# Optimization experiments

Measured on AMD Instinct MI355X. Metric: run time of the kernel, lower is better.

The kernel has to match this reference:

```python
import jax, jax.numpy as jnp
import numpy as np

B, S, U, M = 4096, 64, 128, 32
ODE_UNFOLDS = 6
EPS = 1e-08

def _uniform(k, shape, lo, hi):
    return jax.random.uniform(k, shape, jnp.float32, lo, hi)

def setup_inputs() -> dict:
    key = jax.random.key(0)
    ks = jax.random.split(key, 16)
    return {
        "inputs": jax.random.normal(ks[0], (B, S), jnp.float32),
        "state": jax.random.normal(ks[1], (B, U), jnp.float32),
        "gleak": _uniform(ks[2], (U,), 0.001, 1.0),
        "vleak": _uniform(ks[3], (U,), -0.2, 0.2),
        "cm": _uniform(ks[4], (U,), 0.4, 0.6),
        "sigma": _uniform(ks[5], (U, U), 3.0, 8.0),
        "mu": _uniform(ks[6], (U, U), 0.3, 0.8),
        "w": _uniform(ks[7], (U, U), 0.001, 1.0),
        "erev": jnp.sign(jax.random.normal(ks[8], (U, U), jnp.float32)),
        "sensory_sigma": _uniform(ks[9], (S, U), 3.0, 8.0),
        "sensory_mu": _uniform(ks[10], (S, U), 0.3, 0.8),
        "sensory_w": _uniform(ks[11], (S, U), 0.001, 1.0),
        "sensory_erev": jnp.sign(jax.random.normal(ks[12], (S, U), jnp.float32)),
        "sparsity_mask": (jax.random.uniform(ks[13], (U, U)) < 0.5).astype(jnp.float32),
        "sensory_sparsity_mask": (jax.random.uniform(ks[14], (S, U)) < 0.5).astype(jnp.float32),
        "input_w": jnp.ones((S,), jnp.float32),
        "input_b": jnp.zeros((S,), jnp.float32),
        "output_w": jnp.ones((M,), jnp.float32),
        "output_b": jnp.zeros((M,), jnp.float32),
    }

def reference(inputs, state, gleak, vleak, cm, sigma, mu, w, erev,
              sensory_sigma, sensory_mu, sensory_w, sensory_erev,
              sparsity_mask, sensory_sparsity_mask,
              input_w, input_b, output_w, output_b):
    # input mapping (affine)
    x = inputs * input_w + input_b                       # [B,S]
    # sensory synapse activation: [B,S,U]
    sens_act = (sensory_w * sensory_sparsity_mask) * jax.nn.sigmoid(
        sensory_sigma * (x[:, :, None] - sensory_mu))
    w_num_sensory = jnp.sum(sens_act * sensory_erev, axis=1)   # [B,U]
    w_den_sensory = jnp.sum(sens_act, axis=1)                  # [B,U]

    wm = w * sparsity_mask                                     # masked weights [U,U]
    wme = wm * erev                                            # weights*erev   [U,U]
    cm_t = cm * ODE_UNFOLDS                                    # cm / (1/unfolds)
    leak = gleak * vleak

    v = state
    for _ in range(ODE_UNFOLDS):
        sig = jax.nn.sigmoid(sigma * (v[:, :, None] - mu))     # [B,U,U] (src,dst)
        w_num = jnp.einsum('bsu,su->bu', sig, wme) + w_num_sensory
        w_den = jnp.einsum('bsu,su->bu', sig, wm) + w_den_sensory
        v = (cm_t * v + leak + w_num) / (cm_t + gleak + w_den + EPS)

    out = v[:, :M] * output_w + output_b                       # motor slice + affine
    return out, v
```

## Files before the change

kernel.cpp:

```cpp
#include <hip/hip_runtime.h>
#include <hip/hip_fp16.h>

typedef unsigned short u16;
typedef unsigned int   u32;

#define B_TOTAL 4096
#define ROWS    16
#define NU      128
#define NS      64
#define NM      32
#define UNFOLDS 6
#define LOG2E   1.44269504088896340736f

__device__ __forceinline__ float bf2f(u16 v) {
  return __uint_as_float(((u32)v) << 16);
}
__device__ __forceinline__ u16 f2bf(float f) {
  u32 x = __float_as_uint(f);
  return (u16)((x + 0x7fffu + ((x >> 16) & 1u)) >> 16);
}

template<bool BF16>
__device__ __forceinline__ float LD(const void* p, int i) {
  if (BF16) return bf2f(((const u16*)p)[i]);
  return ((const float*)p)[i];
}

__device__ __forceinline__ float rdlane(float v, int lane) {
  return __int_as_float(__builtin_amdgcn_readlane(__float_as_int(v), lane));
}

__device__ __forceinline__ u32 pk(float a, float b) {
  __half2 h = __halves2half2(__float2half_rn(a), __float2half_rn(b));
  return __builtin_bit_cast(u32, h);
}

__device__ __forceinline__ void step(u32 a0, u32 a1, u32 wv, float vj,
                                     float& n0, float& d0, float& n1, float& d1) {
  float t0, t1, q, aw;
  asm("v_fma_mix_f32 %[t0], %[vj], %[a0], %[a1] op_sel:[0,0,0] op_sel_hi:[0,1,1]\n\t"
      "v_fma_mix_f32 %[t1], %[vj], %[a0], %[a1] op_sel:[0,1,1] op_sel_hi:[0,1,1]\n\t"
      "v_exp_f32 %[t0], %[t0]\n\t"
      "v_exp_f32 %[t1], %[t1]\n\t"
      "v_add_f32 %[t0], 1.0, %[t0]\n\t"
      "v_add_f32 %[t1], 1.0, %[t1]\n\t"
      "v_mul_f32 %[q], %[t0], %[t1]\n\t"
      "v_rcp_f32 %[q], %[q]\n\t"
      "v_and_b32 %[aw], 0x7fff7fff, %[w]\n\t"
      "v_mul_f32 %[t1], %[t1], %[q]\n\t"
      "v_mul_f32 %[t0], %[t0], %[q]\n\t"
      "v_fma_mix_f32 %[n0], %[t1], %[w],  %[n0] op_sel:[0,0,0] op_sel_hi:[0,1,0]\n\t"
      "v_fma_mix_f32 %[d0], %[t1], %[aw], %[d0] op_sel:[0,0,0] op_sel_hi:[0,1,0]\n\t"
      "v_fma_mix_f32 %[n1], %[t0], %[w],  %[n1] op_sel:[0,1,0] op_sel_hi:[0,1,0]\n\t"
      "v_fma_mix_f32 %[d1], %[t0], %[aw], %[d1] op_sel:[0,1,0] op_sel_hi:[0,1,0]"
      : [n0] "+v"(n0), [d0] "+v"(d0), [n1] "+v"(n1), [d1] "+v"(d1),
        [t0] "=&v"(t0), [t1] "=&v"(t1), [q] "=&v"(q), [aw] "=&v"(aw)
      : [vj] "v"(vj), [a0] "v"(a0), [a1] "v"(a1), [w] "v"(wv));
}

template<bool BF16>
__device__ __forceinline__ void body(
    const void* g_in, const void* g_state, const void* g_gleak, const void* g_vleak,
    const void* g_cm, const void* g_sigma, const void* g_mu, const void* g_w,
    const void* g_erev, const void* g_ssig, const void* g_smu, const void* g_sw,
    const void* g_serev, const void* g_mask, const void* g_smask,
    const void* g_iw, const void* g_ib, const void* g_ow, const void* g_ob,
    void* g_out,
    uint2* smA, u32* smW, uint2* smA2, u32* smW2)
{
  const int tid = threadIdx.x;
  const int b0  = blockIdx.x * ROWS;

  #pragma unroll 2
  for (int e = tid; e < NU * 64; e += 1024) {
    int j = e >> 6, l = e & 63;
    int i0 = j * NU + l, i1 = i0 + 64;
    float sl0 = LD<BF16>(g_sigma, i0) * LOG2E, sl1 = LD<BF16>(g_sigma, i1) * LOG2E;
    float ms0 = LD<BF16>(g_mu, i0) * sl0,      ms1 = LD<BF16>(g_mu, i1) * sl1;
    smA[e] = make_uint2(pk(-sl0, -sl1), pk(ms0, ms1));
    float w0 = LD<BF16>(g_w, i0) * LD<BF16>(g_mask, i0) * LD<BF16>(g_erev, i0);
    float w1 = LD<BF16>(g_w, i1) * LD<BF16>(g_mask, i1) * LD<BF16>(g_erev, i1);
    smW[e] = pk(w0, w1);
  }
  #pragma unroll 2
  for (int e = tid; e < NS * 64; e += 1024) {
    int s = e >> 6, l = e & 63;
    int i0 = s * NU + l, i1 = i0 + 64;
    float sl0 = LD<BF16>(g_ssig, i0) * LOG2E, sl1 = LD<BF16>(g_ssig, i1) * LOG2E;
    float ms0 = LD<BF16>(g_smu, i0) * sl0,    ms1 = LD<BF16>(g_smu, i1) * sl1;
    smA2[e] = make_uint2(pk(-sl0, -sl1), pk(ms0, ms1));
    float w0 = LD<BF16>(g_sw, i0) * LD<BF16>(g_smask, i0) * LD<BF16>(g_serev, i0);
    float w1 = LD<BF16>(g_sw, i1) * LD<BF16>(g_smask, i1) * LD<BF16>(g_serev, i1);
    smW2[e] = pk(w0, w1);
  }
  __syncthreads();

  const int r  = tid >> 6;
  const int u0 = tid & 63;
  const int u1 = u0 + 64;
  const int b  = b0 + r;

  float x_lane = LD<BF16>(g_in, b * NS + u0) * LD<BF16>(g_iw, u0) + LD<BF16>(g_ib, u0);
  float v0 = LD<BF16>(g_state, b * NU + u0);
  float v1 = LD<BF16>(g_state, b * NU + u1);
  const float gl0 = LD<BF16>(g_gleak, u0), gl1 = LD<BF16>(g_gleak, u1);
  const float lk0 = gl0 * LD<BF16>(g_vleak, u0);
  const float lk1 = gl1 * LD<BF16>(g_vleak, u1);
  const float cm0 = LD<BF16>(g_cm, u0) * (float)UNFOLDS;
  const float cm1 = LD<BF16>(g_cm, u1) * (float)UNFOLDS;

  const uint2* pA  = smA  + u0;
  const u32*   pW  = smW  + u0;
  const uint2* pA2 = smA2 + u0;
  const u32*   pW2 = smW2 + u0;

  float ns0 = 0.f, ds0 = 0.f, ns1 = 0.f, ds1 = 0.f;
  #pragma unroll 4
  for (int s = 0; s < NS; ++s) {
    float xs = rdlane(x_lane, s);
    uint2 a = pA2[s * 64];
    step(a.x, a.y, pW2[s * 64], xs, ns0, ds0, ns1, ds1);
  }

  #pragma unroll 1
  for (int it = 0; it < UNFOLDS; ++it) {
    float n0 = ns0, d0 = ds0, n1 = ns1, d1 = ds1;
    #pragma unroll 4
    for (int j = 0; j < 64; ++j) {
      float vj = rdlane(v0, j);
      uint2 a = pA[j * 64];
      step(a.x, a.y, pW[j * 64], vj, n0, d0, n1, d1);
    }
    #pragma unroll 4
    for (int j = 0; j < 64; ++j) {
      float vj = rdlane(v1, j);
      uint2 a = pA[(j + 64) * 64];
      step(a.x, a.y, pW[(j + 64) * 64], vj, n0, d0, n1, d1);
    }
    v0 = fmaf(cm0, v0, lk0 + n0) * __builtin_amdgcn_rcpf(cm0 + gl0 + d0 + 1e-8f);
    v1 = fmaf(cm1, v1, lk1 + n1) * __builtin_amdgcn_rcpf(cm1 + gl1 + d1 + 1e-8f);
  }

  if (BF16) {
    u16* om = (u16*)g_out;
    u16* ov = om + B_TOTAL * NM;
    ov[b * NU + u0] = f2bf(v0);
    ov[b * NU + u1] = f2bf(v1);
    if (u0 < NM)
      om[b * NM + u0] = f2bf(fmaf(v0, LD<true>(g_ow, u0), LD<true>(g_ob, u0)));
  } else {
    float* om = (float*)g_out;
    float* ov = om + B_TOTAL * NM;
    ov[b * NU + u0] = v0;
    ov[b * NU + u1] = v1;
    if (u0 < NM)
      om[b * NM + u0] = fmaf(v0, LD<false>(g_ow, u0), LD<false>(g_ob, u0));
  }
}

__global__ __launch_bounds__(1024, 4) void ltc_kernel(
    const void* g_in, const void* g_state, const void* g_gleak, const void* g_vleak,
    const void* g_cm, const void* g_sigma, const void* g_mu, const void* g_w,
    const void* g_erev, const void* g_ssig, const void* g_smu, const void* g_sw,
    const void* g_serev, const void* g_mask, const void* g_smask,
    const void* g_iw, const void* g_ib, const void* g_ow, const void* g_ob,
    void* g_out)
{
  __shared__ uint2 smA [NU * 64];
  __shared__ u32   smW [NU * 64];
  __shared__ uint2 smA2[NS * 64];
  __shared__ u32   smW2[NS * 64];

  const u16* sg = (const u16*)g_sigma;
  int cnt = 0;
  #pragma unroll
  for (int i = 0; i < 32; ++i) {
    float f = bf2f(sg[2 * i]);
    cnt += (f >= 2.0f && f <= 16.0f) ? 1 : 0;
  }
  if (cnt >= 24)
    body<true >(g_in, g_state, g_gleak, g_vleak, g_cm, g_sigma, g_mu, g_w, g_erev,
                g_ssig, g_smu, g_sw, g_serev, g_mask, g_smask,
                g_iw, g_ib, g_ow, g_ob, g_out, smA, smW, smA2, smW2);
  else
    body<false>(g_in, g_state, g_gleak, g_vleak, g_cm, g_sigma, g_mu, g_w, g_erev,
                g_ssig, g_smu, g_sw, g_serev, g_mask, g_smask,
                g_iw, g_ib, g_ow, g_ob, g_out, smA, smW, smA2, smW2);
}

extern "C" void kernel_launch(void* const* d_in, const int* in_sizes, int n_in,
                              void* d_out, int out_size, void* d_ws, size_t ws_size,
                              hipStream_t stream) {
  (void)in_sizes; (void)n_in; (void)out_size; (void)d_ws; (void)ws_size;
  dim3 grid(B_TOTAL / ROWS);
  dim3 block(1024);
  hipLaunchKernelGGL(ltc_kernel, grid, block, 0, stream,
                     d_in[0], d_in[1], d_in[2], d_in[3], d_in[4],
                     d_in[5], d_in[6], d_in[7], d_in[8],
                     d_in[9], d_in[10], d_in[11], d_in[12],
                     d_in[13], d_in[14], d_in[15], d_in[16],
                     d_in[17], d_in[18], d_out);
}
```

Measured before the change: 231.7 us.

## Interleave synapse params into uint4 LDS records and reuse buffer for sensory phase

Packs the slope, offset and weight half2 values of each synapse into one 16-byte LDS record, so each step does a single 128-bit LDS load instead of an 8-byte load plus a 4-byte load. The sensory and recurrent tables now share one buffer: the sensory table is built, consumed, then overwritten by the recurrent table, with an extra barrier between. Unroll factors rise to 8. LDS drops from 144KB to 128KB, though the padding word wastes a quarter of the bandwidth; the sensory compute no longer overlaps the recurrent table build.

```diff
diff --git a/kernel.cpp b/kernel.cpp
--- a/kernel.cpp
+++ b/kernel.cpp
@@ -66,39 +66,27 @@
     const void* g_serev, const void* g_mask, const void* g_smask,
     const void* g_iw, const void* g_ib, const void* g_ow, const void* g_ob,
     void* g_out,
-    uint2* smA, u32* smW, uint2* smA2, u32* smW2)
+    uint4* smR)
 {
   const int tid = threadIdx.x;
   const int b0  = blockIdx.x * ROWS;
 
-  #pragma unroll 2
-  for (int e = tid; e < NU * 64; e += 1024) {
-    int j = e >> 6, l = e & 63;
-    int i0 = j * NU + l, i1 = i0 + 64;
-    float sl0 = LD<BF16>(g_sigma, i0) * LOG2E, sl1 = LD<BF16>(g_sigma, i1) * LOG2E;
-    float ms0 = LD<BF16>(g_mu, i0) * sl0,      ms1 = LD<BF16>(g_mu, i1) * sl1;
-    smA[e] = make_uint2(pk(-sl0, -sl1), pk(ms0, ms1));
-    float w0 = LD<BF16>(g_w, i0) * LD<BF16>(g_mask, i0) * LD<BF16>(g_erev, i0);
-    float w1 = LD<BF16>(g_w, i1) * LD<BF16>(g_mask, i1) * LD<BF16>(g_erev, i1);
-    smW[e] = pk(w0, w1);
-  }
+  const int r  = tid >> 6;
+  const int u0 = tid & 63;
+  const int u1 = u0 + 64;
+  const int b  = b0 + r;
+
   #pragma unroll 2
   for (int e = tid; e < NS * 64; e += 1024) {
     int s = e >> 6, l = e & 63;
     int i0 = s * NU + l, i1 = i0 + 64;
     float sl0 = LD<BF16>(g_ssig, i0) * LOG2E, sl1 = LD<BF16>(g_ssig, i1) * LOG2E;
     float ms0 = LD<BF16>(g_smu, i0) * sl0,    ms1 = LD<BF16>(g_smu, i1) * sl1;
-    smA2[e] = make_uint2(pk(-sl0, -sl1), pk(ms0, ms1));
     float w0 = LD<BF16>(g_sw, i0) * LD<BF16>(g_smask, i0) * LD<BF16>(g_serev, i0);
     float w1 = LD<BF16>(g_sw, i1) * LD<BF16>(g_smask, i1) * LD<BF16>(g_serev, i1);
-    smW2[e] = pk(w0, w1);
+    smR[e] = make_uint4(pk(-sl0, -sl1), pk(ms0, ms1), pk(w0, w1), 0u);
   }
   __syncthreads();
-
-  const int r  = tid >> 6;
-  const int u0 = tid & 63;
-  const int u1 = u0 + 64;
-  const int b  = b0 + r;
 
   float x_lane = LD<BF16>(g_in, b * NS + u0) * LD<BF16>(g_iw, u0) + LD<BF16>(g_ib, u0);
   float v0 = LD<BF16>(g_state, b * NU + u0);
@@ -109,33 +97,43 @@
   const float cm0 = LD<BF16>(g_cm, u0) * (float)UNFOLDS;
   const float cm1 = LD<BF16>(g_cm, u1) * (float)UNFOLDS;
 
-  const uint2* pA  = smA  + u0;
-  const u32*   pW  = smW  + u0;
-  const uint2* pA2 = smA2 + u0;
-  const u32*   pW2 = smW2 + u0;
+  const uint4* pR = smR + u0;
 
   float ns0 = 0.f, ds0 = 0.f, ns1 = 0.f, ds1 = 0.f;
-  #pragma unroll 4
+  #pragma unroll 8
   for (int s = 0; s < NS; ++s) {
     float xs = rdlane(x_lane, s);
-    uint2 a = pA2[s * 64];
-    step(a.x, a.y, pW2[s * 64], xs, ns0, ds0, ns1, ds1);
+    uint4 a = pR[s * 64];
+    step(a.x, a.y, a.z, xs, ns0, ds0, ns1, ds1);
   }
+  __syncthreads();
+
+  #pragma unroll 4
+  for (int e = tid; e < NU * 64; e += 1024) {
+    int j = e >> 6, l = e & 63;
+    int i0 = j * NU + l, i1 = i0 + 64;
+    float sl0 = LD<BF16>(g_sigma, i0) * LOG2E, sl1 = LD<BF16>(g_sigma, i1) * LOG2E;
+    float ms0 = LD<BF16>(g_mu, i0) * sl0,      ms1 = LD<BF16>(g_mu, i1) * sl1;
+    float w0 = LD<BF16>(g_w, i0) * LD<BF16>(g_mask, i0) * LD<BF16>(g_erev, i0);
+    float w1 = LD<BF16>(g_w, i1) * LD<BF16>(g_mask, i1) * LD<BF16>(g_erev, i1);
+    smR[e] = make_uint4(pk(-sl0, -sl1), pk(ms0, ms1), pk(w0, w1), 0u);
+  }
+  __syncthreads();
 
   #pragma unroll 1
   for (int it = 0; it < UNFOLDS; ++it) {
     float n0 = ns0, d0 = ds0, n1 = ns1, d1 = ds1;
-    #pragma unroll 4
+    #pragma unroll 8
     for (int j = 0; j < 64; ++j) {
       float vj = rdlane(v0, j);
-      uint2 a = pA[j * 64];
-      step(a.x, a.y, pW[j * 64], vj, n0, d0, n1, d1);
+      uint4 a = pR[j * 64];
+      step(a.x, a.y, a.z, vj, n0, d0, n1, d1);
     }
-    #pragma unroll 4
+    #pragma unroll 8
     for (int j = 0; j < 64; ++j) {
       float vj = rdlane(v1, j);
-      uint2 a = pA[(j + 64) * 64];
-      step(a.x, a.y, pW[(j + 64) * 64], vj, n0, d0, n1, d1);
+      uint4 a = pR[(j + 64) * 64];
+      step(a.x, a.y, a.z, vj, n0, d0, n1, d1);
     }
     v0 = fmaf(cm0, v0, lk0 + n0) * __builtin_amdgcn_rcpf(cm0 + gl0 + d0 + 1e-8f);
     v1 = fmaf(cm1, v1, lk1 + n1) * __builtin_amdgcn_rcpf(cm1 + gl1 + d1 + 1e-8f);
@@ -166,10 +164,7 @@
     const void* g_iw, const void* g_ib, const void* g_ow, const void* g_ob,
     void* g_out)
 {
-  __shared__ uint2 smA [NU * 64];
-  __shared__ u32   smW [NU * 64];
-  __shared__ uint2 smA2[NS * 64];
-  __shared__ u32   smW2[NS * 64];
+  __shared__ uint4 smR[NU * 64];
 
   const u16* sg = (const u16*)g_sigma;
   int cnt = 0;
@@ -181,11 +176,11 @@
   if (cnt >= 24)
     body<true >(g_in, g_state, g_gleak, g_vleak, g_cm, g_sigma, g_mu, g_w, g_erev,
                 g_ssig, g_smu, g_sw, g_serev, g_mask, g_smask,
-                g_iw, g_ib, g_ow, g_ob, g_out, smA, smW, smA2, smW2);
+                g_iw, g_ib, g_ow, g_ob, g_out, smR);
   else
     body<false>(g_in, g_state, g_gleak, g_vleak, g_cm, g_sigma, g_mu, g_w, g_erev,
                 g_ssig, g_smu, g_sw, g_serev, g_mask, g_smask,
-                g_iw, g_ib, g_ow, g_ob, g_out, smA, smW, smA2, smW2);
+                g_iw, g_ib, g_ow, g_ob, g_out, smR);
 }
 
 extern "C" void kernel_launch(void* const* d_in, const int* in_sizes, int n_in,
```

New measurement: 220.9 us. 4.7% less time.
